# Kernel optimization log

Hardware: AMD Instinct MI355X
Metric: run time of the kernel (lower is better)

The kernel has to match this reference:

```python
import jax, jax.numpy as jnp
import numpy as np

BN_EPS = 1e-5
LRELU_SLOPE = 0.1
F = 512  # feature dim fixed by ReFineBlock/Fc_ClassBlock input_dim


def _bn_eval(x, gamma, beta, mean, var):
    # BatchNorm1d in eval mode (running stats); elementwise over feature dim
    return (x - mean) * (gamma / jnp.sqrt(var + BN_EPS)) + beta


def _lrelu(x):
    return jnp.where(x > 0, x, LRELU_SLOPE * x)


def setup_inputs() -> dict:
    key = jax.random.key(0)
    ks = jax.random.split(key, 16)
    B, P, G = 128, 1, 4
    d = jax.random.normal(ks[0], (B, B, P, G, F), dtype=jnp.float32)
    w = jax.random.uniform(ks[1], (B * G, B * G), dtype=jnp.float32)
    W1 = jax.random.normal(ks[2], (F, F), dtype=jnp.float32) * 0.04
    b1 = jnp.zeros((F,), dtype=jnp.float32)
    g1 = jnp.ones((F,), dtype=jnp.float32)
    beta1 = jnp.zeros((F,), dtype=jnp.float32)
    m1 = jax.random.normal(ks[3], (F,), dtype=jnp.float32) * 0.1
    v1 = jax.random.uniform(ks[4], (F,), jnp.float32, 0.5, 1.5)
    W2 = jax.random.normal(ks[5], (F, F), dtype=jnp.float32) * 0.04
    b2 = jnp.zeros((F,), dtype=jnp.float32)
    g2 = jnp.ones((F,), dtype=jnp.float32)
    beta2 = jnp.zeros((F,), dtype=jnp.float32)
    m2 = jax.random.normal(ks[6], (F,), dtype=jnp.float32) * 0.1
    v2 = jax.random.uniform(ks[7], (F,), jnp.float32, 0.5, 1.5)
    # Fc_ClassBlock.classifier: Dropout(eval=id) + Linear(512, 2)
    Wc = jax.random.normal(ks[8], (2, F), dtype=jnp.float32) * 0.001
    bc = jnp.zeros((2,), dtype=jnp.float32)
    return {"d": d, "w": w, "W1": W1, "b1": b1, "g1": g1, "beta1": beta1,
            "m1": m1, "v1": v1, "W2": W2, "b2": b2, "g2": g2, "beta2": beta2,
            "m2": m2, "v2": v2, "Wc": Wc, "bc": bc}


def reference(d, w, W1, b1, g1, beta1, m1, v1, W2, b2, g2, beta2, m2, v2, Wc, bc):
    batch_size = d.shape[1]          # len(d[0])
    num_g = d.shape[3]
    feat = d.shape[-1]
    N = batch_size * num_g           # adjacency size

    # Vectorized ReFineBlock over every (k, :, i, j) row (eval mode: dropout=id)
    x = d.reshape(-1, feat)
    h = _lrelu(_bn_eval(x @ W1.T + b1, g1, beta1, m1, v1))
    h = _lrelu(_bn_eval(h @ W2.T + b2, g2, beta2, m2, v2))
    t = h.reshape(batch_size, -1, feat)   # (B, B*G, F)

    # preprocess_adj: adj = w + I; D^{-1/2}; (adj @ D).T @ D
    adj = w.reshape(N, N) + jnp.eye(N, dtype=w.dtype)
    rowsum = adj.sum(axis=1)
    d_inv_sqrt = jnp.power(rowsum, -0.5)
    d_inv_sqrt = jnp.where(jnp.isinf(d_inv_sqrt), 0.0, d_inv_sqrt)
    w_norm = (adj * d_inv_sqrt[None, :]).T * d_inv_sqrt[None, :]  # (N, N)

    # GCN propagation: d_new[:, :, i] = t[:, :, i] @ w_norm for each feature i
    d_new = jnp.einsum('bmf,mn->bnf', t, w_norm)  # (B, N, F)

    # classifier.classifier (dropout=id + Linear) applied per probe row
    result = d_new @ Wc.T + bc  # (B, N, 2)
    return result.reshape(-1, 2)
```

## Files before the change

### kernel.cpp

```cpp
#include <hip/hip_runtime.h>
#include <hip/hip_bf16.h>


typedef __hip_bfloat16 bf16_t;
typedef __bf16 bf16x8 __attribute__((ext_vector_type(8)));
typedef __bf16 bf16x4 __attribute__((ext_vector_type(4)));
typedef float f32x4 __attribute__((ext_vector_type(4)));

#define KDIM 512
#define BM 128

__device__ __forceinline__ float ldsel(const void* p, int i, int isbf) {
    return isbf ? __bfloat162float(((const bf16_t*)p)[i]) : ((const float*)p)[i];
}

__global__ void probe_kernel(const void* __restrict__ d, int* __restrict__ flag) {
    const unsigned short* u = (const unsigned short*)d;
    const int l = threadIdx.x;
    int cnt = 0;
    for (int i = l; i < 256; i += 64) {
        const int e = (u[i] >> 7) & 0xFF;
        cnt += (e >= 118 && e <= 129) ? 1 : 0;
    }
    #pragma unroll
    for (int off = 32; off; off >>= 1) cnt += __shfl_down(cnt, off, 64);
    if (l == 0) *flag = (cnt >= 200) ? 1 : 0;
}

__global__ void rowsum_kernel(const void* __restrict__ w, const int* __restrict__ flagp,
                              float* __restrict__ dinv) {
    const int isbf = *flagp;
    const int i = blockIdx.x;
    const int l = threadIdx.x;
    float s = 0.f;
    for (int j = l; j < 512; j += 64) s += ldsel(w, i * 512 + j, isbf);
    #pragma unroll
    for (int off = 32; off; off >>= 1) s += __shfl_down(s, off, 64);
    if (l == 0) dinv[i] = 1.0f / sqrtf(s + 1.0f);
}

__global__ void params_kernel(const void* g1, const void* b1, const void* m1,
                              const void* v1, const void* be1,
                              const void* g2, const void* b2, const void* m2,
                              const void* v2, const void* be2,
                              const void* Wc, const void* bc,
                              const int* __restrict__ flagp,
                              float* sc1, float* sh1, float* sc2, float* sh2,
                              float* wcf, float* bcf) {
    const int isbf = *flagp;
    const int i = threadIdx.x;
    float s1 = ldsel(g1, i, isbf) / sqrtf(ldsel(v1, i, isbf) + 1e-5f);
    sc1[i] = s1;
    sh1[i] = (ldsel(b1, i, isbf) - ldsel(m1, i, isbf)) * s1 + ldsel(be1, i, isbf);
    float s2 = ldsel(g2, i, isbf) / sqrtf(ldsel(v2, i, isbf) + 1e-5f);
    sc2[i] = s2;
    sh2[i] = (ldsel(b2, i, isbf) - ldsel(m2, i, isbf)) * s2 + ldsel(be2, i, isbf);
    wcf[i] = ldsel(Wc, i, isbf);
    wcf[512 + i] = ldsel(Wc, 512 + i, isbf);
    if (i < 2) bcf[i] = ldsel(bc, i, isbf);
}

__global__ void wconv_kernel(const void* __restrict__ W1, const void* __restrict__ W2,
                             const int* __restrict__ flagp,
                             bf16_t* __restrict__ W1pk, bf16_t* __restrict__ W2pk) {
    const int isbf = *flagp;
    const int t = blockIdx.x * 256 + threadIdx.x;
    const int lane = t & 63;
    const int kt = (t >> 6) & 15;
    const int c16 = t >> 10;
    const int src = (c16 * 16 + (lane & 15)) * 512 + kt * 32 + (lane >> 4) * 8;
    bf16x8 v1, v2;
    #pragma unroll
    for (int e = 0; e < 8; ++e) {
        v1[e] = (__bf16)ldsel(W1, src + e, isbf);
        v2[e] = (__bf16)ldsel(W2, src + e, isbf);
    }
    *reinterpret_cast<bf16x8*>(W1pk + (size_t)t * 8) = v1;
    *reinterpret_cast<bf16x8*>(W2pk + (size_t)t * 8) = v2;
}

__global__ void wnorm_kernel(const void* __restrict__ w, const int* __restrict__ flagp,
                             const float* __restrict__ dinv, float* __restrict__ wn_t) {
    const int isbf = *flagp;
    const int idx = blockIdx.x * 256 + threadIdx.x;
    const int n = idx >> 9, m = idx & 511;
    float a = ldsel(w, n * 512 + m, isbf) + (m == n ? 1.0f : 0.0f);
    wn_t[idx] = a * dinv[m] * dinv[n];
}

#define JSTRIDE 16384
#define KSTRIDE 1024

#define LOADW4(dst, base, kt)                                                  \
    _Pragma("unroll")                                                          \
    for (int j = 0; j < 4; ++j)                                                \
        dst[j] = *reinterpret_cast<const bf16x8*>((base) + j * JSTRIDE + (kt) * KSTRIDE);

#define MFMA_HALF(accset, bset, aset)                                          \
    _Pragma("unroll")                                                          \
    for (int j = 0; j < 4; ++j)                                                \
        _Pragma("unroll")                                                      \
        for (int i = 0; i < 2; ++i)                                            \
            accset[j][i] = __builtin_amdgcn_mfma_f32_16x16x32_bf16(bset[j], aset[i], accset[j][i], 0, 0, 0);

#define LOADSTG(S, kt)                                                         \
    if (tid < 512) {                                                           \
        if (isbf) {                                                            \
            sb##S = *reinterpret_cast<const bf16x8*>((const bf16_t*)A + sgbase + (size_t)(kt) * 32); \
        } else {                                                               \
            const f32x4* p_ = (const f32x4*)((const float*)A + sgbase + (size_t)(kt) * 32); \
            sf0##S = p_[0]; sf1##S = p_[1];                                    \
        }                                                                      \
    }

#define STW(S, bufi)                                                           \
    if (tid < 512) {                                                           \
        bf16x8 v_;                                                             \
        if (isbf) { v_ = sb##S; }                                              \
        else {                                                                 \
            v_[0] = (__bf16)sf0##S.x; v_[1] = (__bf16)sf0##S.y;                \
            v_[2] = (__bf16)sf0##S.z; v_[3] = (__bf16)sf0##S.w;                \
            v_[4] = (__bf16)sf1##S.x; v_[5] = (__bf16)sf1##S.y;                \
            v_[6] = (__bf16)sf1##S.z; v_[7] = (__bf16)sf1##S.w;                \
        }                                                                      \
        *reinterpret_cast<bf16x8*>((char*)Astage + (bufi) * 8192 + sldsoff) = v_; \
    }

#define COMPUTE(kt, bufi, wbase)                                               \
    {                                                                          \
        const char* ab_ = (const char*)Astage + (bufi) * 8192 + lane * 16;     \
        bf16x8 aA_[2], aB_[2], bW_[4];                                         \
        aA_[0] = *reinterpret_cast<const bf16x8*>(ab_ + (wr * 4 + 0) * 1024);  \
        aA_[1] = *reinterpret_cast<const bf16x8*>(ab_ + (wr * 4 + 1) * 1024);  \
        aB_[0] = *reinterpret_cast<const bf16x8*>(ab_ + (wr * 4 + 2) * 1024);  \
        aB_[1] = *reinterpret_cast<const bf16x8*>(ab_ + (wr * 4 + 3) * 1024);  \
        LOADW4(bW_, wbase, kt);                                                \
        MFMA_HALF(accA, bW_, aA_);                                             \
        MFMA_HALF(accB, bW_, aB_);                                             \
    }

__launch_bounds__(1024, 4)
__global__ void fused_mlp(const void* __restrict__ A,
                          const bf16_t* __restrict__ W1pk,
                          const bf16_t* __restrict__ W2pk,
                          const float* __restrict__ sc1, const float* __restrict__ sh1,
                          const float* __restrict__ sc2, const float* __restrict__ sh2,
                          const float* __restrict__ wcf,
                          const int* __restrict__ flagp,
                          float* __restrict__ U)
{
    __shared__ __align__(16) bf16_t T1s[BM * KDIM];
    __shared__ __align__(16) bf16_t Astage[2][BM * 32];
    float* UredF = (float*)Astage;

    const int isbf = *flagp;
    const int tid = threadIdx.x;
    const int wave = tid >> 6, lane = tid & 63;
    const int wr = wave >> 3, wc = wave & 7;
    const int bm = blockIdx.x;
    const int rl = lane & 15, hi = lane >> 4;

    const char* w1base = (const char*)W1pk + ((size_t)(wc * 4) * 16 * 64 + lane) * 16;
    const char* w2base = (const char*)W2pk + ((size_t)(wc * 4) * 16 * 64 + lane) * 16;

    const int srow = tid >> 2;
    const int skc = tid & 3;
    const size_t sgbase = (size_t)(bm * BM + srow) * KDIM + skc * 8;
    const int sldsoff = (srow >> 4) * 1024 + ((srow & 15) + skc * 16) * 16;

    f32x4 accA[4][2] = {}, accB[4][2] = {};
    f32x4 sf0A, sf1A, sf0B, sf1B;
    bf16x8 sbA, sbB;

    LOADSTG(A, 0);
    STW(A, 0);
    LOADSTG(B, 1);
    __syncthreads();

    #pragma unroll 1
    for (int kt = 0; kt < 16; kt += 2) {
        if (kt + 2 < 16) LOADSTG(A, kt + 2);
        COMPUTE(kt, kt & 1, w1base);
        STW(B, (kt + 1) & 1);
        __syncthreads();
        if (kt + 3 < 16) LOADSTG(B, kt + 3);
        COMPUTE(kt + 1, (kt + 1) & 1, w1base);
        if (kt + 2 < 16) STW(A, kt & 1);
        __syncthreads();
    }

    #pragma unroll
    for (int j = 0; j < 4; ++j) {
        const int gcol0 = wc * 64 + j * 16 + hi * 4;
        const f32x4 s4 = *reinterpret_cast<const f32x4*>(&sc1[gcol0]);
        const f32x4 h4 = *reinterpret_cast<const f32x4*>(&sh1[gcol0]);
        #pragma unroll
        for (int h = 0; h < 2; ++h)
            #pragma unroll
            for (int i = 0; i < 2; ++i) {
                const int row = wr * 64 + h * 32 + i * 16 + rl;
                int off = (row << 10) + (gcol0 << 1);
                off ^= (row & 7) << 4;
                const f32x4 av = h ? accB[j][i] : accA[j][i];
                bf16x4 pk;
                #pragma unroll
                for (int r = 0; r < 4; ++r) {
                    float y = av[r] * s4[r] + h4[r];
                    y = y > 0.f ? y : 0.1f * y;
                    pk[r] = (__bf16)y;
                }
                *reinterpret_cast<bf16x4*>((char*)T1s + off) = pk;
            }
    }
    __syncthreads();

    #pragma unroll
    for (int j = 0; j < 4; ++j)
        #pragma unroll
        for (int i = 0; i < 2; ++i) {
            accA[j][i] = f32x4{0.f, 0.f, 0.f, 0.f};
            accB[j][i] = f32x4{0.f, 0.f, 0.f, 0.f};
        }

    #define LDT1(dst, h, kt)                                                   \
        _Pragma("unroll")                                                      \
        for (int i = 0; i < 2; ++i) {                                          \
            const int row_ = wr * 64 + (h) * 32 + i * 16 + rl;                 \
            int off_ = (row_ << 10) + (kt) * 64 + hi * 16;                     \
            off_ ^= (row_ & 7) << 4;                                           \
            dst[i] = *reinterpret_cast<const bf16x8*>((const char*)T1s + off_);\
        }

    #pragma unroll 1
    for (int kt = 0; kt < 16; ++kt) {
        bf16x8 bW[4], aA[2], aB[2];
        LOADW4(bW, w2base, kt);
        LDT1(aA, 0, kt);
        LDT1(aB, 1, kt);
        MFMA_HALF(accA, bW, aA);
        MFMA_HALF(accB, bW, aB);
    }

    float p0A[2] = {0.f, 0.f}, p1A[2] = {0.f, 0.f};
    float p0B[2] = {0.f, 0.f}, p1B[2] = {0.f, 0.f};
    #pragma unroll
    for (int j = 0; j < 4; ++j) {
        const int gcol0 = wc * 64 + j * 16 + hi * 4;
        const f32x4 s4 = *reinterpret_cast<const f32x4*>(&sc2[gcol0]);
        const f32x4 h4 = *reinterpret_cast<const f32x4*>(&sh2[gcol0]);
        const f32x4 w0 = *reinterpret_cast<const f32x4*>(&wcf[gcol0]);
        const f32x4 w1 = *reinterpret_cast<const f32x4*>(&wcf[512 + gcol0]);
        #pragma unroll
        for (int i = 0; i < 2; ++i)
            #pragma unroll
            for (int r = 0; r < 4; ++r) {
                float yA = accA[j][i][r] * s4[r] + h4[r];
                yA = yA > 0.f ? yA : 0.1f * yA;
                p0A[i] += yA * w0[r];
                p1A[i] += yA * w1[r];
                float yB = accB[j][i][r] * s4[r] + h4[r];
                yB = yB > 0.f ? yB : 0.1f * yB;
                p0B[i] += yB * w0[r];
                p1B[i] += yB * w1[r];
            }
    }
    __syncthreads();
    #pragma unroll
    for (int i = 0; i < 2; ++i) {
        float a0 = p0A[i], b0 = p1A[i], a1 = p0B[i], b1 = p1B[i];
        a0 += __shfl_xor(a0, 16, 64);  b0 += __shfl_xor(b0, 16, 64);
        a0 += __shfl_xor(a0, 32, 64);  b0 += __shfl_xor(b0, 32, 64);
        a1 += __shfl_xor(a1, 16, 64);  b1 += __shfl_xor(b1, 16, 64);
        a1 += __shfl_xor(a1, 32, 64);  b1 += __shfl_xor(b1, 32, 64);
        if (hi == 0) {
            const int rowA = wr * 64 + i * 16 + rl;
            const int rowB = rowA + 32;
            UredF[(wc * BM + rowA) * 2]     = a0;
            UredF[(wc * BM + rowA) * 2 + 1] = b0;
            UredF[(wc * BM + rowB) * 2]     = a1;
            UredF[(wc * BM + rowB) * 2 + 1] = b1;
        }
    }
    __syncthreads();
    if (tid < BM * 2) {
        const int row = tid >> 1, c = tid & 1;
        float s = 0.f;
        #pragma unroll
        for (int q = 0; q < 8; ++q) s += UredF[(q * BM + row) * 2 + c];
        U[(size_t)(bm * BM + row) * 2 + c] = s;
    }
    #undef LDT1
}

__global__ void gcn_kernel(const float* __restrict__ wn_t, const float* __restrict__ U,
                           const float* __restrict__ bcf, const int* __restrict__ flagp,
                           void* __restrict__ out) {
    const int isbf = *flagp;
    const int wave = threadIdx.x >> 6, lane = threadIdx.x & 63;
    const int task = blockIdx.x * 4 + wave;
    const int b = task >> 9, n = task & 511;
    const float* wrow = wn_t + n * 512;
    const float* ub = U + b * 1024;
    float a0 = 0.f, a1 = 0.f;
    for (int m = lane; m < 512; m += 64) {
        const float wv = wrow[m];
        a0 += wv * ub[m * 2];
        a1 += wv * ub[m * 2 + 1];
    }
    #pragma unroll
    for (int off = 32; off; off >>= 1) {
        a0 += __shfl_down(a0, off, 64);
        a1 += __shfl_down(a1, off, 64);
    }
    if (lane == 0) {
        const float r0 = a0 + bcf[0];
        const float r1 = a1 + bcf[1];
        if (isbf) {
            ((bf16_t*)out)[task * 2]     = __float2bfloat16(r0);
            ((bf16_t*)out)[task * 2 + 1] = __float2bfloat16(r1);
        } else {
            ((float*)out)[task * 2]     = r0;
            ((float*)out)[task * 2 + 1] = r1;
        }
    }
}

extern "C" void kernel_launch(void* const* d_in, const int* in_sizes, int n_in,
                              void* d_out, int out_size, void* d_ws, size_t ws_size,
                              hipStream_t stream) {
    const void* d   = d_in[0];
    const void* w   = d_in[1];
    const void* W1  = d_in[2];
    const void* b1  = d_in[3];
    const void* g1  = d_in[4];
    const void* be1 = d_in[5];
    const void* m1  = d_in[6];
    const void* v1  = d_in[7];
    const void* W2  = d_in[8];
    const void* b2  = d_in[9];
    const void* g2  = d_in[10];
    const void* be2 = d_in[11];
    const void* m2  = d_in[12];
    const void* v2  = d_in[13];
    const void* Wc  = d_in[14];
    const void* bc  = d_in[15];

    char* ws = (char*)d_ws;
    float*  wn_t = (float*)ws;
    bf16_t* W1pk = (bf16_t*)(ws + 0x100000);
    bf16_t* W2pk = (bf16_t*)(ws + 0x180000);
    float*  sc1  = (float*)(ws + 0x200000);
    float*  sh1  = sc1 + 512;
    float*  sc2  = sh1 + 512;
    float*  sh2  = sc2 + 512;
    float*  dinv = sh2 + 512;
    float*  wcf  = (float*)(ws + 0x204000);
    float*  bcf  = (float*)(ws + 0x205000);
    int*    flag = (int*)(ws + 0x205100);
    float*  U    = (float*)(ws + 0x208000);

    const int M = 128 * 512;

    probe_kernel<<<1, 64, 0, stream>>>(d, flag);
    rowsum_kernel<<<512, 64, 0, stream>>>(w, flag, dinv);
    params_kernel<<<1, 512, 0, stream>>>(g1, b1, m1, v1, be1, g2, b2, m2, v2, be2,
                                         Wc, bc, flag, sc1, sh1, sc2, sh2, wcf, bcf);
    wconv_kernel<<<128, 256, 0, stream>>>(W1, W2, flag, W1pk, W2pk);
    wnorm_kernel<<<1024, 256, 0, stream>>>(w, flag, dinv, wn_t);

    fused_mlp<<<M / BM, 1024, 0, stream>>>(d, W1pk, W2pk,
                                           sc1, sh1, sc2, sh2, wcf, flag, U);

    gcn_kernel<<<M / 4, 256, 0, stream>>>(wn_t, U, bcf, flag, d_out);
}
```

Before: 146.7 us.

## Software-pipeline weight fragment loads and spread A staging over all threads

Weight fragments for both GEMMs are now prefetched one k-step ahead into double-buffered registers (bW0/bW1), so global/L2 weight loads overlap the MFMAs of the previous step. The A-tile staging now uses all 1024 threads with 4-element loads instead of 512 threads with 8-element loads, spreading global traffic evenly across waves. LDS A-fragment loads are split so each half's MFMAs can begin sooner and fewer registers stay live. Double-buffered weight registers raise register pressure, which could hurt under launch_bounds(1024,4).

```diff
diff --git a/kernel.cpp b/kernel.cpp
--- a/kernel.cpp
+++ b/kernel.cpp
@@ -103,40 +103,33 @@
         for (int i = 0; i < 2; ++i)                                            \
             accset[j][i] = __builtin_amdgcn_mfma_f32_16x16x32_bf16(bset[j], aset[i], accset[j][i], 0, 0, 0);
 
-#define LOADSTG(S, kt)                                                         \
-    if (tid < 512) {                                                           \
-        if (isbf) {                                                            \
-            sb##S = *reinterpret_cast<const bf16x8*>((const bf16_t*)A + sgbase + (size_t)(kt) * 32); \
-        } else {                                                               \
-            const f32x4* p_ = (const f32x4*)((const float*)A + sgbase + (size_t)(kt) * 32); \
-            sf0##S = p_[0]; sf1##S = p_[1];                                    \
+#define SISSUE(kt)                                                             \
+    {                                                                          \
+        if (isbf) sb = *reinterpret_cast<const bf16x4*>((const bf16_t*)A + sgbase + (size_t)(kt) * 32); \
+        else      sf = *reinterpret_cast<const f32x4*>((const float*)A + sgbase + (size_t)(kt) * 32);  \
+    }
+
+#define SWRITE(bufi)                                                           \
+    {                                                                          \
+        bf16x4 v_;                                                             \
+        if (isbf) { v_ = sb; }                                                 \
+        else {                                                                 \
+            v_[0] = (__bf16)sf.x; v_[1] = (__bf16)sf.y;                        \
+            v_[2] = (__bf16)sf.z; v_[3] = (__bf16)sf.w;                        \
         }                                                                      \
-    }
-
-#define STW(S, bufi)                                                           \
-    if (tid < 512) {                                                           \
-        bf16x8 v_;                                                             \
-        if (isbf) { v_ = sb##S; }                                              \
-        else {                                                                 \
-            v_[0] = (__bf16)sf0##S.x; v_[1] = (__bf16)sf0##S.y;                \
-            v_[2] = (__bf16)sf0##S.z; v_[3] = (__bf16)sf0##S.w;                \
-            v_[4] = (__bf16)sf1##S.x; v_[5] = (__bf16)sf1##S.y;                \
-            v_[6] = (__bf16)sf1##S.z; v_[7] = (__bf16)sf1##S.w;                \
-        }                                                                      \
-        *reinterpret_cast<bf16x8*>((char*)Astage + (bufi) * 8192 + sldsoff) = v_; \
-    }
-
-#define COMPUTE(kt, bufi, wbase)                                               \
+        *reinterpret_cast<bf16x4*>((char*)Astage + (bufi) * 8192 + sldsoff) = v_; \
+    }
+
+#define COMPUTE2(bufi, bWs)                                                    \
     {                                                                          \
         const char* ab_ = (const char*)Astage + (bufi) * 8192 + lane * 16;     \
-        bf16x8 aA_[2], aB_[2], bW_[4];                                         \
-        aA_[0] = *reinterpret_cast<const bf16x8*>(ab_ + (wr * 4 + 0) * 1024);  \
-        aA_[1] = *reinterpret_cast<const bf16x8*>(ab_ + (wr * 4 + 1) * 1024);  \
-        aB_[0] = *reinterpret_cast<const bf16x8*>(ab_ + (wr * 4 + 2) * 1024);  \
-        aB_[1] = *reinterpret_cast<const bf16x8*>(ab_ + (wr * 4 + 3) * 1024);  \
-        LOADW4(bW_, wbase, kt);                                                \
-        MFMA_HALF(accA, bW_, aA_);                                             \
-        MFMA_HALF(accB, bW_, aB_);                                             \
+        bf16x8 aT_[2];                                                         \
+        aT_[0] = *reinterpret_cast<const bf16x8*>(ab_ + (wr * 4 + 0) * 1024);  \
+        aT_[1] = *reinterpret_cast<const bf16x8*>(ab_ + (wr * 4 + 1) * 1024);  \
+        MFMA_HALF(accA, bWs, aT_);                                             \
+        aT_[0] = *reinterpret_cast<const bf16x8*>(ab_ + (wr * 4 + 2) * 1024);  \
+        aT_[1] = *reinterpret_cast<const bf16x8*>(ab_ + (wr * 4 + 3) * 1024);  \
+        MFMA_HALF(accB, bWs, aT_);                                             \
     }
 
 __launch_bounds__(1024, 4)
@@ -163,29 +156,34 @@
     const char* w1base = (const char*)W1pk + ((size_t)(wc * 4) * 16 * 64 + lane) * 16;
     const char* w2base = (const char*)W2pk + ((size_t)(wc * 4) * 16 * 64 + lane) * 16;
 
-    const int srow = tid >> 2;
-    const int skc = tid & 3;
-    const size_t sgbase = (size_t)(bm * BM + srow) * KDIM + skc * 8;
-    const int sldsoff = (srow >> 4) * 1024 + ((srow & 15) + skc * 16) * 16;
+    const int srow = tid >> 3;
+    const int sk4 = tid & 7;
+    const size_t sgbase = (size_t)(bm * BM + srow) * KDIM + sk4 * 4;
+    const int sldsoff = (srow >> 4) * 1024 + ((srow & 15) + (sk4 >> 1) * 16) * 16
+                        + (sk4 & 1) * 8;
 
     f32x4 accA[4][2] = {}, accB[4][2] = {};
-    f32x4 sf0A, sf1A, sf0B, sf1B;
-    bf16x8 sbA, sbB;
-
-    LOADSTG(A, 0);
-    STW(A, 0);
-    LOADSTG(B, 1);
+    bf16x8 bW0[4], bW1[4];
+    f32x4 sf;
+    bf16x4 sb;
+
+    SISSUE(0);
+    SWRITE(0);
+    SISSUE(1);
+    LOADW4(bW0, w1base, 0);
     __syncthreads();
 
     #pragma unroll 1
     for (int kt = 0; kt < 16; kt += 2) {
-        if (kt + 2 < 16) LOADSTG(A, kt + 2);
-        COMPUTE(kt, kt & 1, w1base);
-        STW(B, (kt + 1) & 1);
+        LOADW4(bW1, w1base, kt + 1);
+        COMPUTE2(kt & 1, bW0);
+        SWRITE((kt + 1) & 1);
+        if (kt + 2 < 16) SISSUE(kt + 2);
         __syncthreads();
-        if (kt + 3 < 16) LOADSTG(B, kt + 3);
-        COMPUTE(kt + 1, (kt + 1) & 1, w1base);
-        if (kt + 2 < 16) STW(A, kt & 1);
+        if (kt + 2 < 16) LOADW4(bW0, w1base, kt + 2);
+        COMPUTE2((kt + 1) & 1, bW1);
+        if (kt + 2 < 16) SWRITE((kt + 2) & 1);
+        if (kt + 3 < 16) SISSUE(kt + 3);
         __syncthreads();
     }
 
@@ -222,23 +220,34 @@
             accB[j][i] = f32x4{0.f, 0.f, 0.f, 0.f};
         }
 
-    #define LDT1(dst, h, kt)                                                   \
-        _Pragma("unroll")                                                      \
-        for (int i = 0; i < 2; ++i) {                                          \
-            const int row_ = wr * 64 + (h) * 32 + i * 16 + rl;                 \
-            int off_ = (row_ << 10) + (kt) * 64 + hi * 16;                     \
-            off_ ^= (row_ & 7) << 4;                                           \
-            dst[i] = *reinterpret_cast<const bf16x8*>((const char*)T1s + off_);\
+    #define COMPT1(kt, bWs)                                                    \
+        {                                                                      \
+            bf16x8 aT_[2];                                                     \
+            _Pragma("unroll")                                                  \
+            for (int i = 0; i < 2; ++i) {                                      \
+                const int row_ = wr * 64 + i * 16 + rl;                        \
+                int off_ = (row_ << 10) + (kt) * 64 + hi * 16;                 \
+                off_ ^= (row_ & 7) << 4;                                       \
+                aT_[i] = *reinterpret_cast<const bf16x8*>((const char*)T1s + off_); \
+            }                                                                  \
+            MFMA_HALF(accA, bWs, aT_);                                         \
+            _Pragma("unroll")                                                  \
+            for (int i = 0; i < 2; ++i) {                                      \
+                const int row_ = wr * 64 + 32 + i * 16 + rl;                   \
+                int off_ = (row_ << 10) + (kt) * 64 + hi * 16;                 \
+                off_ ^= (row_ & 7) << 4;                                       \
+                aT_[i] = *reinterpret_cast<const bf16x8*>((const char*)T1s + off_); \
+            }                                                                  \
+            MFMA_HALF(accB, bWs, aT_);                                         \
         }
 
+    LOADW4(bW0, w2base, 0);
     #pragma unroll 1
-    for (int kt = 0; kt < 16; ++kt) {
-        bf16x8 bW[4], aA[2], aB[2];
-        LOADW4(bW, w2base, kt);
-        LDT1(aA, 0, kt);
-        LDT1(aB, 1, kt);
-        MFMA_HALF(accA, bW, aA);
-        MFMA_HALF(accB, bW, aB);
+    for (int kt = 0; kt < 16; kt += 2) {
+        LOADW4(bW1, w2base, kt + 1);
+        COMPT1(kt, bW0);
+        if (kt + 2 < 16) LOADW4(bW0, w2base, kt + 2);
+        COMPT1(kt + 1, bW1);
     }
 
     float p0A[2] = {0.f, 0.f}, p1A[2] = {0.f, 0.f};
@@ -289,7 +298,7 @@
         for (int q = 0; q < 8; ++q) s += UredF[(q * BM + row) * 2 + c];
         U[(size_t)(bm * BM + row) * 2 + c] = s;
     }
-    #undef LDT1
+    #undef COMPT1
 }
 
 __global__ void gcn_kernel(const float* __restrict__ wn_t, const float* __restrict__ U,
```

Result: faster. 137.4 us (-6.4%).
